# Kernel optimization log

Hardware: AMD Instinct MI355X
Metric: run time of the kernel (lower is better)

## Reference

```python
import jax, jax.numpy as jnp
import numpy as np

# 3 blocks x dilations [1..128] -> 24 residual layers, receptive field ~765
DILATIONS = tuple([1, 2, 4, 8, 16, 32, 64, 128] * 3)
WAVEFORM_BITS = 8


def setup_inputs() -> dict:
    key = jax.random.key(0)
    ks = jax.random.split(key, 8)
    B, C, S, K = 64, 64, 256, 256
    L = len(DILATIONS)
    s = 0.1  # keep gated activations away from saturation
    return {
        "waveform_seed": jax.random.randint(ks[0], (B, 1, 1), 0, K, dtype=jnp.int32),
        "embed": jax.random.normal(ks[1], (K, C), jnp.float32) * s,
        "conv_k": jax.random.normal(ks[2], (L, 2, C, 2 * C), jnp.float32) * s,  # [layer, tap(last/cur), C_in, 2C]
        "conv_b": jnp.zeros((L, 2 * C), jnp.float32),
        "res_w": jax.random.normal(ks[3], (L, C, C), jnp.float32) * s,
        "res_b": jnp.zeros((L, C), jnp.float32),
        "skip_w": jax.random.normal(ks[4], (L, C, S), jnp.float32) * s,
        "skip_b": jnp.zeros((L, S), jnp.float32),
        "out0_w": jax.random.normal(ks[5], (S, K), jnp.float32) * s,
        "out0_b": jnp.zeros((K,), jnp.float32),
        "out1_w": jax.random.normal(ks[6], (K, K), jnp.float32) * s,
        "out1_b": jnp.zeros((K,), jnp.float32),
        "max_infer_samples": 128,
    }


def _generate(seed, embed, conv_k, conv_b, res_w, res_b, skip_w, skip_b,
              out0_w, out0_b, out1_w, out1_b, T):
    B = seed.shape[0]
    C = embed.shape[1]
    sample0 = seed.reshape(B)
    # one circular-buffer queue per layer, length = dilation rate, zero-initialized
    queues0 = tuple(jnp.zeros((d, B, C), embed.dtype) for d in DILATIONS)

    def body(carry, _):
        t, sample, queues = carry
        x_cur = embed[sample]  # [B, C] embedding lookup of previous sample
        skip_sum = jnp.zeros((B, skip_w.shape[-1]), embed.dtype)
        new_queues = []
        for i, d in enumerate(DILATIONS):
            q = queues[i]
            pos = t % d  # circular buffer position == queue pop(0)/append semantics
            x_last = q[pos]
            new_queues.append(q.at[pos].set(x_cur))
            # kernel-size-2 dilated causal conv at a single step == two GEMMs
            h = x_last @ conv_k[i, 0] + x_cur @ conv_k[i, 1] + conv_b[i]  # [B, 2C]
            g = jnp.tanh(h[:, :C]) * jax.nn.sigmoid(h[:, C:])  # gated activation
            x_cur = x_cur + g @ res_w[i] + res_b[i]  # residual out
            skip_sum = skip_sum + g @ skip_w[i] + skip_b[i]  # skip connection
        h0 = jax.nn.relu(skip_sum @ out0_w + out0_b)
        logits = h0 @ out1_w + out1_b  # [B, K]
        nxt = jnp.argmax(logits, axis=-1).astype(jnp.int32)  # deterministic sampling
        return (t + 1, nxt, tuple(new_queues)), (nxt, logits)

    _, (samples, logits) = jax.lax.scan(
        body, (jnp.int32(0), sample0, queues0), None, length=T)
    return samples.transpose(1, 0), logits.transpose(1, 0, 2)  # [B,T], [B,T,K]


def reference(waveform_seed, embed, conv_k, conv_b, res_w, res_b, skip_w, skip_b,
              out0_w, out0_b, out1_w, out1_b, max_infer_samples):
    samples, logits = _generate(waveform_seed, embed, conv_k, conv_b, res_w, res_b,
                                skip_w, skip_b, out0_w, out0_b, out1_w, out1_b,
                                max_infer_samples)
    K = embed.shape[0]
    miu = float(K - 1)
    # rev quantize: map class in [0, 2^bits-1] back to [-1, 1]
    miu_wav = 2.0 * samples.astype(jnp.float32) / (2.0 ** WAVEFORM_BITS - 1.0) - 1.0
    # rev mu-law companding
    pred_wav = jnp.sign(miu_wav) * ((1.0 + miu) ** jnp.abs(miu_wav) - 1.0) / miu
    return pred_wav, logits
```

## Files before the change

### kernel.cpp

```cpp
#include <hip/hip_runtime.h>
#include <math.h>

#define NL 24
#define NB 64
#define TPB 512
#define QROWS 765
#define QFLOATS ((size_t)NB * QROWS * 64)
#define PACKW_F4 ((size_t)NL * 8 * 18 * 64)

typedef float vf4 __attribute__((ext_vector_type(4)));

struct WBc  { float4 v[8];  };
struct WBrs { float4 v[10]; };

__device__ __forceinline__ float hadd4(float4 v) { return (v.x + v.y) + (v.z + v.w); }
__device__ __forceinline__ void fma4(float4& a, float4 x, float4 w) {
    a.x = fmaf(x.x, w.x, a.x); a.y = fmaf(x.y, w.y, a.y);
    a.z = fmaf(x.z, w.z, a.z); a.w = fmaf(x.w, w.w, a.w);
}

__device__ __forceinline__ void bar() {
    asm volatile("s_waitcnt lgkmcnt(0)" ::: "memory");
    __builtin_amdgcn_s_barrier();
    asm volatile("" ::: "memory");
}

__device__ __forceinline__ void pf_c(WBc& b, const float4* __restrict__ packW, int i, int w, int l) {
    const float4* p = packW + ((size_t)(i * 8 + w) * 18) * 64 + l;
#pragma unroll
    for (int j = 0; j < 8; ++j) b.v[j] = p[j * 64];
}
__device__ __forceinline__ void pf_rs(WBrs& b, const float4* __restrict__ packW, int i, int w, int l) {
    const float4* p = packW + ((size_t)(i * 8 + w) * 18) * 64 + l;
#pragma unroll
    for (int j = 0; j < 10; ++j) b.v[j] = p[(8 + j) * 64];
}

__global__ void repack(const float* __restrict__ conv_k, const float* __restrict__ res_w,
                       const float* __restrict__ skip_w, const float* __restrict__ out0_w,
                       const float* __restrict__ out1_w, float* __restrict__ ws) {
    const int l = threadIdx.x;
    const int bb = blockIdx.x;
    float4* packW = (float4*)(ws + QFLOATS);
    float4* packH = packW + PACKW_F4;
    if (bb < NL * 8) {
        const int i = bb >> 3, w = bb & 7;
        float4* dst = packW + (size_t)bb * 18 * 64 + l;
        const int c  = w * 8 + (l & 7);
        const int kb = (l >> 3) * 16;
#pragma unroll
        for (int j = 0; j < 4; ++j) {
            float4 v;
            int k0 = kb + j * 4;
            v.x = conv_k[(((size_t)i * 2 + ((k0+0) >> 6)) * 64 + ((k0+0) & 63)) * 128 + c];
            v.y = conv_k[(((size_t)i * 2 + ((k0+1) >> 6)) * 64 + ((k0+1) & 63)) * 128 + c];
            v.z = conv_k[(((size_t)i * 2 + ((k0+2) >> 6)) * 64 + ((k0+2) & 63)) * 128 + c];
            v.w = conv_k[(((size_t)i * 2 + ((k0+3) >> 6)) * 64 + ((k0+3) & 63)) * 128 + c];
            dst[j * 64] = v;
        }
#pragma unroll
        for (int j = 0; j < 4; ++j) {
            float4 v;
            int k0 = kb + j * 4; int c2 = c + 64;
            v.x = conv_k[(((size_t)i * 2 + ((k0+0) >> 6)) * 64 + ((k0+0) & 63)) * 128 + c2];
            v.y = conv_k[(((size_t)i * 2 + ((k0+1) >> 6)) * 64 + ((k0+1) & 63)) * 128 + c2];
            v.z = conv_k[(((size_t)i * 2 + ((k0+2) >> 6)) * 64 + ((k0+2) & 63)) * 128 + c2];
            v.w = conv_k[(((size_t)i * 2 + ((k0+3) >> 6)) * 64 + ((k0+3) & 63)) * 128 + c2];
            dst[(4 + j) * 64] = v;
        }
        const int kr = (l >> 3) * 8;
#pragma unroll
        for (int j = 0; j < 2; ++j) {
            float4 v; int k0 = kr + j * 4;
            v.x = res_w[((size_t)i * 64 + k0 + 0) * 64 + c];
            v.y = res_w[((size_t)i * 64 + k0 + 1) * 64 + c];
            v.z = res_w[((size_t)i * 64 + k0 + 2) * 64 + c];
            v.w = res_w[((size_t)i * 64 + k0 + 3) * 64 + c];
            dst[(8 + j) * 64] = v;
        }
        const int s0 = w * 32 + (l & 15) * 2;
        const int ks = (l >> 4) * 16;
#pragma unroll
        for (int j = 0; j < 4; ++j) {
            float4 v; int k0 = ks + j * 4;
            v.x = skip_w[((size_t)i * 64 + k0 + 0) * 256 + s0];
            v.y = skip_w[((size_t)i * 64 + k0 + 1) * 256 + s0];
            v.z = skip_w[((size_t)i * 64 + k0 + 2) * 256 + s0];
            v.w = skip_w[((size_t)i * 64 + k0 + 3) * 256 + s0];
            dst[(10 + j) * 64] = v;
        }
#pragma unroll
        for (int j = 0; j < 4; ++j) {
            float4 v; int k0 = ks + j * 4; int s1 = s0 + 1;
            v.x = skip_w[((size_t)i * 64 + k0 + 0) * 256 + s1];
            v.y = skip_w[((size_t)i * 64 + k0 + 1) * 256 + s1];
            v.z = skip_w[((size_t)i * 64 + k0 + 2) * 256 + s1];
            v.w = skip_w[((size_t)i * 64 + k0 + 3) * 256 + s1];
            dst[(14 + j) * 64] = v;
        }
    } else {
        const int hb = bb - NL * 8;
        const int which = hb >> 3, w = hb & 7;
        const float* W = which ? out1_w : out0_w;
        float4* dst = packH + (size_t)hb * 32 * 64 + l;
        const int c  = w * 32 + (l & 31);
        const int kb = (l >> 5) * 128;
        for (int j = 0; j < 32; ++j) {
            float4 v; int k0 = kb + j * 4;
            v.x = W[(size_t)(k0 + 0) * 256 + c];
            v.y = W[(size_t)(k0 + 1) * 256 + c];
            v.z = W[(size_t)(k0 + 2) * 256 + c];
            v.w = W[(size_t)(k0 + 3) * 256 + c];
            dst[j * 64] = v;
        }
    }
}

__global__ __launch_bounds__(TPB, 1)
void wavenet_gen(const int* __restrict__ seed,
                 const float* __restrict__ embed,
                 const float* __restrict__ conv_b,
                 const float* __restrict__ res_b,
                 const float* __restrict__ skip_b,
                 const float* __restrict__ out0_b,
                 const float* __restrict__ out1_b,
                 const int* __restrict__ Tptr,
                 float* __restrict__ out,
                 float* __restrict__ ring,
                 const float4* __restrict__ packW,
                 const float4* __restrict__ packH)
{
    const int b   = blockIdx.x;
    const int tid = threadIdx.x;
    const int w   = tid >> 6;
    const int l   = tid & 63;
    const int T   = *Tptr;

    __shared__ __align__(16) float x2[128];
    __shared__ __align__(16) float gg[64];
    __shared__ __align__(16) float sk_lds[256];
    __shared__ __align__(16) float h0_lds[256];
    __shared__ __align__(16) float ebt[256 * 64];
    __shared__ __align__(16) float cb[NL * 128];
    __shared__ __align__(16) float rb[NL * 64];
    __shared__ __align__(16) float o0b[256], o1b[256];
    __shared__ __align__(16) float sbt[256];
    __shared__ float wmaxv[8];
    __shared__ int   wmaxi[8];

    float* q = ring + (size_t)b * (QROWS * 64);

    {
        vf4* q4 = (vf4*)q;
        const vf4 z = (vf4){0.f, 0.f, 0.f, 0.f};
        for (int idx = tid; idx < QROWS * 64 / 4; idx += TPB)
            __builtin_nontemporal_store(z, &q4[idx]);
        const float4* s4; float4* d4;
        s4 = (const float4*)embed;  d4 = (float4*)ebt;
        for (int idx = tid; idx < 256 * 64 / 4; idx += TPB) d4[idx] = s4[idx];
        s4 = (const float4*)conv_b; d4 = (float4*)cb;
        for (int idx = tid; idx < NL * 128 / 4; idx += TPB) d4[idx] = s4[idx];
        s4 = (const float4*)res_b;  d4 = (float4*)rb;
        for (int idx = tid; idx < NL * 64 / 4; idx += TPB) d4[idx] = s4[idx];
        s4 = (const float4*)out0_b; d4 = (float4*)o0b;
        for (int idx = tid; idx < 64; idx += TPB) d4[idx] = s4[idx];
        s4 = (const float4*)out1_b; d4 = (float4*)o1b;
        for (int idx = tid; idx < 64; idx += TPB) d4[idx] = s4[idx];
        if (tid < 256) {
            float acc = 0.f;
            for (int i = 0; i < NL; ++i) acc += skip_b[i * 256 + tid];
            sbt[tid] = acc;
        }
    }
    __syncthreads();
    if (tid < 64) {
        x2[tid] = 0.f;
        const int smp = seed[b];
        x2[64 + tid] = ebt[smp * 64 + tid];
    }
    __syncthreads();

    WBc  C0, C1;
    WBrs RS;
    pf_c(C0, packW, 0, w, l);

    float* out_pred = out + (size_t)b * T;
    float* out_log  = out + (size_t)NB * T + (size_t)b * T * 256;

    const int c   = w * 8 + (l & 7);
    const int kb  = (l >> 3) * 16;
    const int kr  = (l >> 3) * 8;
    const int ks  = (l >> 4) * 16;
    const int s0  = w * 32 + (l & 15) * 2;
    const int c2  = w * 32 + (l & 31);
    const int kb2 = (l >> 5) * 128;

    for (int t = 0; t < T; ++t) {
        float skv0 = 0.f, skv1 = 0.f;

        auto layer = [&](WBc& cur, WBc& nxt, const int i) {
            const int inx = (i + 1 < NL) ? (i + 1) : 0;
            pf_rs(RS, packW, i, w, l);
            pf_c(nxt, packW, inx, w, l);
            float xlnext = 0.f;
            if (w == 7) {
                const int d2 = 1 << (inx & 7);
                const int row2 = 255 * (inx >> 3) + (d2 - 1) + (t & (d2 - 1));
                xlnext = __builtin_nontemporal_load(&q[(size_t)row2 * 64 + l]);
            }
            if (w == 6) {
                const int d = 1 << (i & 7);
                const int row = 255 * (i >> 3) + (d - 1) + (t & (d - 1));
                __builtin_nontemporal_store(x2[64 + l], &q[(size_t)row * 64 + l]);
            }
            float4 xk0 = *(const float4*)&x2[kb];
            float4 xk1 = *(const float4*)&x2[kb + 4];
            float4 xk2 = *(const float4*)&x2[kb + 8];
            float4 xk3 = *(const float4*)&x2[kb + 12];
            float4 aA = make_float4(0.f, 0.f, 0.f, 0.f);
            float4 aB = make_float4(0.f, 0.f, 0.f, 0.f);
            fma4(aA, xk0, cur.v[0]); fma4(aA, xk1, cur.v[1]);
            fma4(aA, xk2, cur.v[2]); fma4(aA, xk3, cur.v[3]);
            fma4(aB, xk0, cur.v[4]); fma4(aB, xk1, cur.v[5]);
            fma4(aB, xk2, cur.v[6]); fma4(aB, xk3, cur.v[7]);
            float hA = hadd4(aA), hB = hadd4(aB);
            hA += __shfl_xor(hA, 8);  hB += __shfl_xor(hB, 8);
            hA += __shfl_xor(hA, 16); hB += __shfl_xor(hB, 16);
            hA += __shfl_xor(hA, 32); hB += __shfl_xor(hB, 32);
            hA += cb[i * 128 + c];
            hB += cb[i * 128 + 64 + c];
            const float g = tanhf(hA) * (1.f / (1.f + expf(-hB)));
            if (l < 8) gg[w * 8 + l] = g;
            bar();
            float4 gr0 = *(const float4*)&gg[kr];
            float4 gr1 = *(const float4*)&gg[kr + 4];
            float4 ra = make_float4(0.f, 0.f, 0.f, 0.f);
            fma4(ra, gr0, RS.v[0]); fma4(ra, gr1, RS.v[1]);
            float racc = hadd4(ra);
            racc += __shfl_xor(racc, 8);
            racc += __shfl_xor(racc, 16);
            racc += __shfl_xor(racc, 32);
            const float xnew = x2[64 + c] + racc + rb[i * 64 + c];
            float4 gs0 = *(const float4*)&gg[ks];
            float4 gs1 = *(const float4*)&gg[ks + 4];
            float4 gs2 = *(const float4*)&gg[ks + 8];
            float4 gs3 = *(const float4*)&gg[ks + 12];
            float4 sa0 = make_float4(0.f, 0.f, 0.f, 0.f);
            float4 sa1 = make_float4(0.f, 0.f, 0.f, 0.f);
            fma4(sa0, gs0, RS.v[2]); fma4(sa0, gs1, RS.v[3]);
            fma4(sa0, gs2, RS.v[4]); fma4(sa0, gs3, RS.v[5]);
            fma4(sa1, gs0, RS.v[6]); fma4(sa1, gs1, RS.v[7]);
            fma4(sa1, gs2, RS.v[8]); fma4(sa1, gs3, RS.v[9]);
            float ss0 = hadd4(sa0), ss1 = hadd4(sa1);
            ss0 += __shfl_xor(ss0, 16); ss1 += __shfl_xor(ss1, 16);
            ss0 += __shfl_xor(ss0, 32); ss1 += __shfl_xor(ss1, 32);
            skv0 += ss0;
            skv1 += ss1;
            if (l < 8) x2[64 + w * 8 + l] = xnew;
            if (w == 7) x2[l] = xlnext;
            bar();
        };

#pragma unroll 1
        for (int ii = 0; ii < NL; ii += 2) {
            layer(C0, C1, ii);
            layer(C1, C0, ii + 1);
        }

        if (l < 16) { sk_lds[s0] = skv0 + sbt[s0]; sk_lds[s0 + 1] = skv1 + sbt[s0 + 1]; }
        bar();
        {
            const float4* hp = packH + ((size_t)w * 32) * 64 + l;
            float4 ha = make_float4(0.f, 0.f, 0.f, 0.f);
#pragma unroll 8
            for (int cc = 0; cc < 32; ++cc) {
                float4 wv = hp[cc * 64];
                float4 sv = *(const float4*)&sk_lds[kb2 + cc * 4];
                fma4(ha, sv, wv);
            }
            float hs = hadd4(ha);
            hs += __shfl_xor(hs, 32);
            const float h0 = fmaxf(hs + o0b[c2], 0.f);
            if (l < 32) h0_lds[c2] = h0;
        }
        bar();
        float logit;
        {
            const float4* hp = packH + ((size_t)(8 + w) * 32) * 64 + l;
            float4 la = make_float4(0.f, 0.f, 0.f, 0.f);
#pragma unroll 8
            for (int cc = 0; cc < 32; ++cc) {
                float4 wv = hp[cc * 64];
                float4 hv = *(const float4*)&h0_lds[kb2 + cc * 4];
                fma4(la, hv, wv);
            }
            float ls = hadd4(la);
            ls += __shfl_xor(ls, 32);
            logit = ls + o1b[c2];
            if (l < 32)
                __builtin_nontemporal_store(logit, &out_log[(size_t)t * 256 + c2]);
        }
        {
            float bv = logit; int bi = c2;
#pragma unroll
            for (int off = 1; off <= 16; off <<= 1) {
                const float ov = __shfl_xor(bv, off);
                const int   oi = __shfl_xor(bi, off);
                if (ov > bv || (ov == bv && oi < bi)) { bv = ov; bi = oi; }
            }
            if (l == 0) { wmaxv[w] = bv; wmaxi[w] = bi; }
        }
        bar();
        {
            float fv = wmaxv[0]; int fi = wmaxi[0];
#pragma unroll
            for (int ww = 1; ww < 8; ++ww) {
                const float vv = wmaxv[ww]; const int vi = wmaxi[ww];
                if (vv > fv || (vv == fv && vi < fi)) { fv = vv; fi = vi; }
            }
            if (tid < 64) x2[64 + tid] = ebt[fi * 64 + tid];
            if (tid == 0) {
                const float mw = (float)fi * (2.0f / 255.0f) - 1.0f;
                const float a  = fabsf(mw);
                const float p  = (exp2f(8.0f * a) - 1.0f) * (1.0f / 255.0f);
                __builtin_nontemporal_store((mw < 0.f) ? -p : p, &out_pred[t]);
            }
        }
        bar();
    }
}

extern "C" void kernel_launch(void* const* d_in, const int* in_sizes, int n_in,
                              void* d_out, int out_size, void* d_ws, size_t ws_size,
                              hipStream_t stream) {
    const int*   seed   = (const int*)  d_in[0];
    const float* embed  = (const float*)d_in[1];
    const float* conv_k = (const float*)d_in[2];
    const float* conv_b = (const float*)d_in[3];
    const float* res_w  = (const float*)d_in[4];
    const float* res_b  = (const float*)d_in[5];
    const float* skip_w = (const float*)d_in[6];
    const float* skip_b = (const float*)d_in[7];
    const float* out0_w = (const float*)d_in[8];
    const float* out0_b = (const float*)d_in[9];
    const float* out1_w = (const float*)d_in[10];
    const float* out1_b = (const float*)d_in[11];
    const int*   Tptr   = (const int*)  d_in[12];

    float* ws = (float*)d_ws;
    float* ring = ws;
    const float4* packW = (const float4*)(ws + QFLOATS);
    const float4* packH = packW + PACKW_F4;

    repack<<<dim3(NL * 8 + 16), dim3(64), 0, stream>>>(
        conv_k, res_w, skip_w, out0_w, out1_w, ws);

    wavenet_gen<<<dim3(NB), dim3(TPB), 0, stream>>>(
        seed, embed, conv_b, res_b, skip_b, out0_b, out1_b, Tptr,
        (float*)d_out, ring, packW, packH);
}
```

Baseline: 6.379 ms.

## Fold residual projection into next layer's conv to halve per-layer barriers

```diff
diff --git a/kernel.cpp b/kernel.cpp
--- a/kernel.cpp
+++ b/kernel.cpp
@@ -5,12 +5,16 @@
 #define NB 64
 #define TPB 512
 #define QROWS 765
-#define QFLOATS ((size_t)NB * QROWS * 64)
-#define PACKW_F4 ((size_t)NL * 8 * 18 * 64)
+#define RING_F  3133440
+#define MB_OFF  RING_F
+#define CB2_OFF (MB_OFF + 24*64*128)
+#define CV_OFF  (CB2_OFF + 24*128)
+#define RS_OFF  (CV_OFF + 24*512*48)
+#define PH_OFF  (RS_OFF + 24*512*40)
 
 typedef float vf4 __attribute__((ext_vector_type(4)));
 
-struct WBc  { float4 v[8];  };
+struct WBc  { float4 v[12]; };
 struct WBrs { float4 v[10]; };
 
 __device__ __forceinline__ float hadd4(float4 v) { return (v.x + v.y) + (v.z + v.w); }
@@ -18,95 +22,128 @@
     a.x = fmaf(x.x, w.x, a.x); a.y = fmaf(x.y, w.y, a.y);
     a.z = fmaf(x.z, w.z, a.z); a.w = fmaf(x.w, w.w, a.w);
 }
-
 __device__ __forceinline__ void bar() {
     asm volatile("s_waitcnt lgkmcnt(0)" ::: "memory");
     __builtin_amdgcn_s_barrier();
     asm volatile("" ::: "memory");
 }
-
-__device__ __forceinline__ void pf_c(WBc& b, const float4* __restrict__ packW, int i, int w, int l) {
-    const float4* p = packW + ((size_t)(i * 8 + w) * 18) * 64 + l;
-#pragma unroll
-    for (int j = 0; j < 8; ++j) b.v[j] = p[j * 64];
-}
-__device__ __forceinline__ void pf_rs(WBrs& b, const float4* __restrict__ packW, int i, int w, int l) {
-    const float4* p = packW + ((size_t)(i * 8 + w) * 18) * 64 + l;
-#pragma unroll
-    for (int j = 0; j < 10; ++j) b.v[j] = p[(8 + j) * 64];
-}
-
-__global__ void repack(const float* __restrict__ conv_k, const float* __restrict__ res_w,
-                       const float* __restrict__ skip_w, const float* __restrict__ out0_w,
-                       const float* __restrict__ out1_w, float* __restrict__ ws) {
-    const int l = threadIdx.x;
-    const int bb = blockIdx.x;
-    float4* packW = (float4*)(ws + QFLOATS);
-    float4* packH = packW + PACKW_F4;
-    if (bb < NL * 8) {
-        const int i = bb >> 3, w = bb & 7;
-        float4* dst = packW + (size_t)bb * 18 * 64 + l;
+__device__ __forceinline__ void pf_cv(WBc& b, const float4* __restrict__ cvp, int layer, int tid) {
+    const float4* p = cvp + (size_t)layer * (12 * 512) + tid;
+#pragma unroll
+    for (int j = 0; j < 12; ++j) b.v[j] = p[j * 512];
+}
+__device__ __forceinline__ void pf_rs(WBrs& b, const float4* __restrict__ rsp, int layer, int tid) {
+    const float4* p = rsp + (size_t)layer * (10 * 512) + tid;
+#pragma unroll
+    for (int j = 0; j < 10; ++j) b.v[j] = p[j * 512];
+}
+
+__global__ void repack1(const float* __restrict__ conv_k, const float* __restrict__ res_w,
+                        const float* __restrict__ conv_b, const float* __restrict__ res_b,
+                        float* __restrict__ ws) {
+    const int i = blockIdx.x, col = threadIdx.x;
+    float* M   = ws + MB_OFF;
+    float* cb2 = ws + CB2_OFF;
+    if (i == 0) {
+        for (int m = 0; m < 64; ++m) M[(size_t)m * 128 + col] = 0.f;
+        cb2[col] = conv_b[col];
+        return;
+    }
+    float k1[64];
+#pragma unroll
+    for (int k = 0; k < 64; ++k)
+        k1[k] = conv_k[((size_t)(i * 2 + 1) * 64 + k) * 128 + col];
+    for (int m = 0; m < 64; ++m) {
+        float a = 0.f;
+#pragma unroll
+        for (int k = 0; k < 64; ++k)
+            a = fmaf(res_w[((size_t)(i - 1) * 64 + m) * 64 + k], k1[k], a);
+        M[((size_t)i * 64 + m) * 128 + col] = a;
+    }
+    float cb = conv_b[i * 128 + col];
+#pragma unroll
+    for (int k = 0; k < 64; ++k)
+        cb = fmaf(res_b[(i - 1) * 64 + k], k1[k], cb);
+    cb2[i * 128 + col] = cb;
+}
+
+__global__ void repack2(const float* __restrict__ conv_k, const float* __restrict__ res_w,
+                        const float* __restrict__ skip_w, const float* __restrict__ out0_w,
+                        const float* __restrict__ out1_w, float* __restrict__ ws) {
+    const int bb = blockIdx.x, tid = threadIdx.x;
+    float4* CV = (float4*)(ws + CV_OFF);
+    float4* RS = (float4*)(ws + RS_OFF);
+    float4* PH = (float4*)(ws + PH_OFF);
+    const float* M = ws + MB_OFF;
+    if (bb < NL) {
+        const int i = bb, w = tid >> 6, l = tid & 63;
         const int c  = w * 8 + (l & 7);
-        const int kb = (l >> 3) * 16;
-#pragma unroll
-        for (int j = 0; j < 4; ++j) {
-            float4 v;
-            int k0 = kb + j * 4;
-            v.x = conv_k[(((size_t)i * 2 + ((k0+0) >> 6)) * 64 + ((k0+0) & 63)) * 128 + c];
-            v.y = conv_k[(((size_t)i * 2 + ((k0+1) >> 6)) * 64 + ((k0+1) & 63)) * 128 + c];
-            v.z = conv_k[(((size_t)i * 2 + ((k0+2) >> 6)) * 64 + ((k0+2) & 63)) * 128 + c];
-            v.w = conv_k[(((size_t)i * 2 + ((k0+3) >> 6)) * 64 + ((k0+3) & 63)) * 128 + c];
-            dst[j * 64] = v;
-        }
-#pragma unroll
-        for (int j = 0; j < 4; ++j) {
-            float4 v;
-            int k0 = kb + j * 4; int c2 = c + 64;
-            v.x = conv_k[(((size_t)i * 2 + ((k0+0) >> 6)) * 64 + ((k0+0) & 63)) * 128 + c2];
-            v.y = conv_k[(((size_t)i * 2 + ((k0+1) >> 6)) * 64 + ((k0+1) & 63)) * 128 + c2];
-            v.z = conv_k[(((size_t)i * 2 + ((k0+2) >> 6)) * 64 + ((k0+2) & 63)) * 128 + c2];
-            v.w = conv_k[(((size_t)i * 2 + ((k0+3) >> 6)) * 64 + ((k0+3) & 63)) * 128 + c2];
-            dst[(4 + j) * 64] = v;
-        }
-        const int kr = (l >> 3) * 8;
-#pragma unroll
-        for (int j = 0; j < 2; ++j) {
-            float4 v; int k0 = kr + j * 4;
-            v.x = res_w[((size_t)i * 64 + k0 + 0) * 64 + c];
-            v.y = res_w[((size_t)i * 64 + k0 + 1) * 64 + c];
-            v.z = res_w[((size_t)i * 64 + k0 + 2) * 64 + c];
-            v.w = res_w[((size_t)i * 64 + k0 + 3) * 64 + c];
-            dst[(8 + j) * 64] = v;
+        const int k0 = (l >> 3) * 8;
+        float4* dst = CV + (size_t)i * (12 * 512) + tid;
+#pragma unroll
+        for (int half = 0; half < 2; ++half) {
+            const int cc = c + half * 64;
+#pragma unroll
+            for (int jj = 0; jj < 2; ++jj) {
+                const int kk = k0 + jj * 4;
+                float4 a, b, m;
+                a.x = conv_k[((size_t)(i * 2 + 0) * 64 + kk + 0) * 128 + cc];
+                a.y = conv_k[((size_t)(i * 2 + 0) * 64 + kk + 1) * 128 + cc];
+                a.z = conv_k[((size_t)(i * 2 + 0) * 64 + kk + 2) * 128 + cc];
+                a.w = conv_k[((size_t)(i * 2 + 0) * 64 + kk + 3) * 128 + cc];
+                b.x = conv_k[((size_t)(i * 2 + 1) * 64 + kk + 0) * 128 + cc];
+                b.y = conv_k[((size_t)(i * 2 + 1) * 64 + kk + 1) * 128 + cc];
+                b.z = conv_k[((size_t)(i * 2 + 1) * 64 + kk + 2) * 128 + cc];
+                b.w = conv_k[((size_t)(i * 2 + 1) * 64 + kk + 3) * 128 + cc];
+                m.x = M[((size_t)i * 64 + kk + 0) * 128 + cc];
+                m.y = M[((size_t)i * 64 + kk + 1) * 128 + cc];
+                m.z = M[((size_t)i * 64 + kk + 2) * 128 + cc];
+                m.w = M[((size_t)i * 64 + kk + 3) * 128 + cc];
+                dst[(half * 6 + 0 + jj) * 512] = a;
+                dst[(half * 6 + 2 + jj) * 512] = b;
+                dst[(half * 6 + 4 + jj) * 512] = m;
+            }
+        }
+        float4* rdst = RS + (size_t)i * (10 * 512) + tid;
+#pragma unroll
+        for (int jj = 0; jj < 2; ++jj) {
+            float4 v; const int kk = k0 + jj * 4;
+            v.x = res_w[((size_t)i * 64 + kk + 0) * 64 + c];
+            v.y = res_w[((size_t)i * 64 + kk + 1) * 64 + c];
+            v.z = res_w[((size_t)i * 64 + kk + 2) * 64 + c];
+            v.w = res_w[((size_t)i * 64 + kk + 3) * 64 + c];
+            rdst[jj * 512] = v;
         }
         const int s0 = w * 32 + (l & 15) * 2;
         const int ks = (l >> 4) * 16;
 #pragma unroll
-        for (int j = 0; j < 4; ++j) {
-            float4 v; int k0 = ks + j * 4;
-            v.x = skip_w[((size_t)i * 64 + k0 + 0) * 256 + s0];
-            v.y = skip_w[((size_t)i * 64 + k0 + 1) * 256 + s0];
-            v.z = skip_w[((size_t)i * 64 + k0 + 2) * 256 + s0];
-            v.w = skip_w[((size_t)i * 64 + k0 + 3) * 256 + s0];
-            dst[(10 + j) * 64] = v;
-        }
-#pragma unroll
-        for (int j = 0; j < 4; ++j) {
-            float4 v; int k0 = ks + j * 4; int s1 = s0 + 1;
-            v.x = skip_w[((size_t)i * 64 + k0 + 0) * 256 + s1];
-            v.y = skip_w[((size_t)i * 64 + k0 + 1) * 256 + s1];
-            v.z = skip_w[((size_t)i * 64 + k0 + 2) * 256 + s1];
-            v.w = skip_w[((size_t)i * 64 + k0 + 3) * 256 + s1];
-            dst[(14 + j) * 64] = v;
+        for (int jj = 0; jj < 4; ++jj) {
+            float4 v; const int kk = ks + jj * 4;
+            v.x = skip_w[((size_t)i * 64 + kk + 0) * 256 + s0];
+            v.y = skip_w[((size_t)i * 64 + kk + 1) * 256 + s0];
+            v.z = skip_w[((size_t)i * 64 + kk + 2) * 256 + s0];
+            v.w = skip_w[((size_t)i * 64 + kk + 3) * 256 + s0];
+            rdst[(2 + jj) * 512] = v;
+        }
+#pragma unroll
+        for (int jj = 0; jj < 4; ++jj) {
+            float4 v; const int kk = ks + jj * 4; const int s1 = s0 + 1;
+            v.x = skip_w[((size_t)i * 64 + kk + 0) * 256 + s1];
+            v.y = skip_w[((size_t)i * 64 + kk + 1) * 256 + s1];
+            v.z = skip_w[((size_t)i * 64 + kk + 2) * 256 + s1];
+            v.w = skip_w[((size_t)i * 64 + kk + 3) * 256 + s1];
+            rdst[(6 + jj) * 512] = v;
         }
     } else {
-        const int hb = bb - NL * 8;
-        const int which = hb >> 3, w = hb & 7;
+        if (tid >= 64) return;
+        const int hb = bb - NL;
+        const int which = hb >> 3, w = hb & 7, l = tid;
         const float* W = which ? out1_w : out0_w;
-        float4* dst = packH + (size_t)hb * 32 * 64 + l;
+        float4* dst = PH + (size_t)hb * (32 * 64) + l;
         const int c  = w * 32 + (l & 31);
         const int kb = (l >> 5) * 128;
         for (int j = 0; j < 32; ++j) {
-            float4 v; int k0 = kb + j * 4;
+            float4 v; const int k0 = kb + j * 4;
             v.x = W[(size_t)(k0 + 0) * 256 + c];
             v.y = W[(size_t)(k0 + 1) * 256 + c];
             v.z = W[(size_t)(k0 + 2) * 256 + c];
@@ -119,7 +156,6 @@
 __global__ __launch_bounds__(TPB, 1)
 void wavenet_gen(const int* __restrict__ seed,
                  const float* __restrict__ embed,
-                 const float* __restrict__ conv_b,
                  const float* __restrict__ res_b,
                  const float* __restrict__ skip_b,
                  const float* __restrict__ out0_b,
@@ -127,8 +163,10 @@
                  const int* __restrict__ Tptr,
                  float* __restrict__ out,
                  float* __restrict__ ring,
-                 const float4* __restrict__ packW,
-                 const float4* __restrict__ packH)
+                 const float4* __restrict__ cvp,
+                 const float4* __restrict__ rsp,
+                 const float4* __restrict__ php,
+                 const float* __restrict__ cb2p)
 {
     const int b   = blockIdx.x;
     const int tid = threadIdx.x;
@@ -136,15 +174,15 @@
     const int l   = tid & 63;
     const int T   = *Tptr;
 
-    __shared__ __align__(16) float x2[128];
-    __shared__ __align__(16) float gg[64];
-    __shared__ __align__(16) float sk_lds[256];
-    __shared__ __align__(16) float h0_lds[256];
+    __shared__ __align__(16) float xl[2][64];
+    __shared__ __align__(16) float yb[2][64];
+    __shared__ __align__(16) float gb[2][64];
+    __shared__ __align__(16) float skl[256];
+    __shared__ __align__(16) float h0l[256];
     __shared__ __align__(16) float ebt[256 * 64];
-    __shared__ __align__(16) float cb[NL * 128];
-    __shared__ __align__(16) float rb[NL * 64];
-    __shared__ __align__(16) float o0b[256], o1b[256];
-    __shared__ __align__(16) float sbt[256];
+    __shared__ __align__(16) float cb2S[NL * 128];
+    __shared__ __align__(16) float rbS[NL * 64];
+    __shared__ __align__(16) float o0bS[256], o1bS[256], sbtS[256];
     __shared__ float wmaxv[8];
     __shared__ int   wmaxi[8];
 
@@ -158,93 +196,132 @@
         const float4* s4; float4* d4;
         s4 = (const float4*)embed;  d4 = (float4*)ebt;
         for (int idx = tid; idx < 256 * 64 / 4; idx += TPB) d4[idx] = s4[idx];
-        s4 = (const float4*)conv_b; d4 = (float4*)cb;
+        s4 = (const float4*)cb2p;   d4 = (float4*)cb2S;
         for (int idx = tid; idx < NL * 128 / 4; idx += TPB) d4[idx] = s4[idx];
-        s4 = (const float4*)res_b;  d4 = (float4*)rb;
+        s4 = (const float4*)res_b;  d4 = (float4*)rbS;
         for (int idx = tid; idx < NL * 64 / 4; idx += TPB) d4[idx] = s4[idx];
-        s4 = (const float4*)out0_b; d4 = (float4*)o0b;
+        s4 = (const float4*)out0_b; d4 = (float4*)o0bS;
         for (int idx = tid; idx < 64; idx += TPB) d4[idx] = s4[idx];
-        s4 = (const float4*)out1_b; d4 = (float4*)o1b;
+        s4 = (const float4*)out1_b; d4 = (float4*)o1bS;
         for (int idx = tid; idx < 64; idx += TPB) d4[idx] = s4[idx];
         if (tid < 256) {
             float acc = 0.f;
             for (int i = 0; i < NL; ++i) acc += skip_b[i * 256 + tid];
-            sbt[tid] = acc;
+            sbtS[tid] = acc;
         }
     }
     __syncthreads();
     if (tid < 64) {
-        x2[tid] = 0.f;
         const int smp = seed[b];
-        x2[64 + tid] = ebt[smp * 64 + tid];
+        yb[0][tid] = ebt[smp * 64 + tid];
+        yb[1][tid] = 0.f;
+        xl[0][tid] = 0.f;
+        xl[1][tid] = 0.f;
+        gb[0][tid] = 0.f;
+        gb[1][tid] = 0.f;
     }
     __syncthreads();
 
-    WBc  C0, C1;
+    WBc  CVa, CVb;
     WBrs RS;
-    pf_c(C0, packW, 0, w, l);
+    pf_cv(CVa, cvp, 0, tid);
 
     float* out_pred = out + (size_t)b * T;
     float* out_log  = out + (size_t)NB * T + (size_t)b * T * 256;
 
     const int c   = w * 8 + (l & 7);
-    const int kb  = (l >> 3) * 16;
-    const int kr  = (l >> 3) * 8;
+    const int k0  = (l >> 3) * 8;
     const int ks  = (l >> 4) * 16;
     const int s0  = w * 32 + (l & 15) * 2;
     const int c2  = w * 32 + (l & 31);
     const int kb2 = (l >> 5) * 128;
 
+    float skv0 = 0.f, skv1 = 0.f;
+
     for (int t = 0; t < T; ++t) {
-        float skv0 = 0.f, skv1 = 0.f;
-
-        auto layer = [&](WBc& cur, WBc& nxt, const int i) {
-            const int inx = (i + 1 < NL) ? (i + 1) : 0;
-            pf_rs(RS, packW, i, w, l);
-            pf_c(nxt, packW, inx, w, l);
-            float xlnext = 0.f;
+
+        auto phase = [&](WBc& cur, WBc& nxt, const int i) {
+            const int j = (i + 1 < NL) ? (i + 1) : 0;
+            float xln = 0.f;
             if (w == 7) {
-                const int d2 = 1 << (inx & 7);
-                const int row2 = 255 * (inx >> 3) + (d2 - 1) + (t & (d2 - 1));
-                xlnext = __builtin_nontemporal_load(&q[(size_t)row2 * 64 + l]);
-            }
-            if (w == 6) {
-                const int d = 1 << (i & 7);
-                const int row = 255 * (i >> 3) + (d - 1) + (t & (d - 1));
-                __builtin_nontemporal_store(x2[64 + l], &q[(size_t)row * 64 + l]);
-            }
-            float4 xk0 = *(const float4*)&x2[kb];
-            float4 xk1 = *(const float4*)&x2[kb + 4];
-            float4 xk2 = *(const float4*)&x2[kb + 8];
-            float4 xk3 = *(const float4*)&x2[kb + 12];
+                const int dj = 1 << (j & 7);
+                const int s  = (i == NL - 1) ? (t + 1) : t;
+                const int row = 255 * (j >> 3) + (dj - 1) + (s & (dj - 1));
+                xln = __builtin_nontemporal_load(&q[(size_t)row * 64 + l]);
+            }
+            if (i) pf_rs(RS, rsp, i - 1, tid);
+            pf_cv(nxt, cvp, j, tid);
+            if (w == 6 && i) {
+                const int dp = 1 << ((i - 1) & 7);
+                const int row = 255 * ((i - 1) >> 3) + (dp - 1) + (t & (dp - 1));
+                __builtin_nontemporal_store(yb[(i - 1) & 1][l], &q[(size_t)row * 64 + l]);
+            }
+            const int ybi = i ? ((i - 1) & 1) : 0;
+            const int gbi = (i - 1) & 1;
+            const float4 xl0 = *(const float4*)&xl[i & 1][k0];
+            const float4 xl1 = *(const float4*)&xl[i & 1][k0 + 4];
+            const float4 yp0 = *(const float4*)&yb[ybi][k0];
+            const float4 yp1 = *(const float4*)&yb[ybi][k0 + 4];
+            const float4 gp0 = *(const float4*)&gb[gbi][k0];
+            const float4 gp1 = *(const float4*)&gb[gbi][k0 + 4];
             float4 aA = make_float4(0.f, 0.f, 0.f, 0.f);
             float4 aB = make_float4(0.f, 0.f, 0.f, 0.f);
-            fma4(aA, xk0, cur.v[0]); fma4(aA, xk1, cur.v[1]);
-            fma4(aA, xk2, cur.v[2]); fma4(aA, xk3, cur.v[3]);
-            fma4(aB, xk0, cur.v[4]); fma4(aB, xk1, cur.v[5]);
-            fma4(aB, xk2, cur.v[6]); fma4(aB, xk3, cur.v[7]);
+            fma4(aA, xl0, cur.v[0]); fma4(aA, xl1, cur.v[1]);
+            fma4(aA, yp0, cur.v[2]); fma4(aA, yp1, cur.v[3]);
+            fma4(aA, gp0, cur.v[4]); fma4(aA, gp1, cur.v[5]);
+            fma4(aB, xl0, cur.v[6]); fma4(aB, xl1, cur.v[7]);
+            fma4(aB, yp0, cur.v[8]); fma4(aB, yp1, cur.v[9]);
+            fma4(aB, gp0, cur.v[10]); fma4(aB, gp1, cur.v[11]);
             float hA = hadd4(aA), hB = hadd4(aB);
             hA += __shfl_xor(hA, 8);  hB += __shfl_xor(hB, 8);
             hA += __shfl_xor(hA, 16); hB += __shfl_xor(hB, 16);
             hA += __shfl_xor(hA, 32); hB += __shfl_xor(hB, 32);
-            hA += cb[i * 128 + c];
-            hB += cb[i * 128 + 64 + c];
+            hA += cb2S[i * 128 + c];
+            hB += cb2S[i * 128 + 64 + c];
             const float g = tanhf(hA) * (1.f / (1.f + expf(-hB)));
-            if (l < 8) gg[w * 8 + l] = g;
+            float ynew = 0.f;
+            if (i) {
+                float4 ra = make_float4(0.f, 0.f, 0.f, 0.f);
+                fma4(ra, gp0, RS.v[0]); fma4(ra, gp1, RS.v[1]);
+                float racc = hadd4(ra);
+                racc += __shfl_xor(racc, 8);
+                racc += __shfl_xor(racc, 16);
+                racc += __shfl_xor(racc, 32);
+                ynew = yb[ybi][c] + racc + rbS[(i - 1) * 64 + c];
+                const float4 gs0 = *(const float4*)&gb[gbi][ks];
+                const float4 gs1 = *(const float4*)&gb[gbi][ks + 4];
+                const float4 gs2 = *(const float4*)&gb[gbi][ks + 8];
+                const float4 gs3 = *(const float4*)&gb[gbi][ks + 12];
+                float4 sa0 = make_float4(0.f, 0.f, 0.f, 0.f);
+                float4 sa1 = make_float4(0.f, 0.f, 0.f, 0.f);
+                fma4(sa0, gs0, RS.v[2]); fma4(sa0, gs1, RS.v[3]);
+                fma4(sa0, gs2, RS.v[4]); fma4(sa0, gs3, RS.v[5]);
+                fma4(sa1, gs0, RS.v[6]); fma4(sa1, gs1, RS.v[7]);
+                fma4(sa1, gs2, RS.v[8]); fma4(sa1, gs3, RS.v[9]);
+                float ss0 = hadd4(sa0), ss1 = hadd4(sa1);
+                ss0 += __shfl_xor(ss0, 16); ss1 += __shfl_xor(ss1, 16);
+                ss0 += __shfl_xor(ss0, 32); ss1 += __shfl_xor(ss1, 32);
+                skv0 += ss0;
+                skv1 += ss1;
+            }
+            if (l < 8) gb[i & 1][w * 8 + l] = g;
+            if (i && l < 8) yb[i & 1][w * 8 + l] = ynew;
+            if (w == 7) xl[j & 1][l] = xln;
             bar();
-            float4 gr0 = *(const float4*)&gg[kr];
-            float4 gr1 = *(const float4*)&gg[kr + 4];
-            float4 ra = make_float4(0.f, 0.f, 0.f, 0.f);
-            fma4(ra, gr0, RS.v[0]); fma4(ra, gr1, RS.v[1]);
-            float racc = hadd4(ra);
-            racc += __shfl_xor(racc, 8);
-            racc += __shfl_xor(racc, 16);
-            racc += __shfl_xor(racc, 32);
-            const float xnew = x2[64 + c] + racc + rb[i * 64 + c];
-            float4 gs0 = *(const float4*)&gg[ks];
-            float4 gs1 = *(const float4*)&gg[ks + 4];
-            float4 gs2 = *(const float4*)&gg[ks + 8];
-            float4 gs3 = *(const float4*)&gg[ks + 12];
+        };
+
+#pragma unroll 1
+        for (int ii = 0; ii < NL; ii += 2) {
+            phase(CVa, CVb, ii);
+            phase(CVb, CVa, ii + 1);
+        }
+
+        {
+            pf_rs(RS, rsp, NL - 1, tid);
+            const float4 gs0 = *(const float4*)&gb[1][ks];
+            const float4 gs1 = *(const float4*)&gb[1][ks + 4];
+            const float4 gs2 = *(const float4*)&gb[1][ks + 8];
+            const float4 gs3 = *(const float4*)&gb[1][ks + 12];
             float4 sa0 = make_float4(0.f, 0.f, 0.f, 0.f);
             float4 sa1 = make_float4(0.f, 0.f, 0.f, 0.f);
             fma4(sa0, gs0, RS.v[2]); fma4(sa0, gs1, RS.v[3]);
@@ -256,51 +333,46 @@
             ss0 += __shfl_xor(ss0, 32); ss1 += __shfl_xor(ss1, 32);
             skv0 += ss0;
             skv1 += ss1;
-            if (l < 8) x2[64 + w * 8 + l] = xnew;
-            if (w == 7) x2[l] = xlnext;
+            if (l < 16) {
+                skl[s0] = skv0 + sbtS[s0];
+                skl[s0 + 1] = skv1 + sbtS[s0 + 1];
+            }
+            skv0 = 0.f; skv1 = 0.f;
+            if (w == 6) {
+                const int row = 510 + 127 + (t & 127);
+                __builtin_nontemporal_store(yb[1][l], &q[(size_t)row * 64 + l]);
+            }
             bar();
-        };
-
-#pragma unroll 1
-        for (int ii = 0; ii < NL; ii += 2) {
-            layer(C0, C1, ii);
-            layer(C1, C0, ii + 1);
-        }
-
-        if (l < 16) { sk_lds[s0] = skv0 + sbt[s0]; sk_lds[s0 + 1] = skv1 + sbt[s0 + 1]; }
-        bar();
+        }
         {
-            const float4* hp = packH + ((size_t)w * 32) * 64 + l;
+            const float4* hp = php + ((size_t)w * 32) * 64 + l;
             float4 ha = make_float4(0.f, 0.f, 0.f, 0.f);
 #pragma unroll 8
             for (int cc = 0; cc < 32; ++cc) {
                 float4 wv = hp[cc * 64];
-                float4 sv = *(const float4*)&sk_lds[kb2 + cc * 4];
+                float4 sv = *(const float4*)&skl[kb2 + cc * 4];
                 fma4(ha, sv, wv);
             }
             float hs = hadd4(ha);
             hs += __shfl_xor(hs, 32);
-            const float h0 = fmaxf(hs + o0b[c2], 0.f);
-            if (l < 32) h0_lds[c2] = h0;
+            const float h0 = fmaxf(hs + o0bS[c2], 0.f);
+            if (l < 32) h0l[c2] = h0;
         }
         bar();
-        float logit;
         {
-            const float4* hp = packH + ((size_t)(8 + w) * 32) * 64 + l;
+            const float4* hp = php + ((size_t)(8 + w) * 32) * 64 + l;
             float4 la = make_float4(0.f, 0.f, 0.f, 0.f);
 #pragma unroll 8
             for (int cc = 0; cc < 32; ++cc) {
                 float4 wv = hp[cc * 64];
-                float4 hv = *(const float4*)&h0_lds[kb2 + cc * 4];
+                float4 hv = *(const float4*)&h0l[kb2 + cc * 4];
                 fma4(la, hv, wv);
             }
             float ls = hadd4(la);
             ls += __shfl_xor(ls, 32);
-            logit = ls + o1b[c2];
+            const float logit = ls + o1bS[c2];
             if (l < 32)
                 __builtin_nontemporal_store(logit, &out_log[(size_t)t * 256 + c2]);
-        }
-        {
             float bv = logit; int bi = c2;
 #pragma unroll
             for (int off = 1; off <= 16; off <<= 1) {
@@ -318,7 +390,7 @@
                 const float vv = wmaxv[ww]; const int vi = wmaxi[ww];
                 if (vv > fv || (vv == fv && vi < fi)) { fv = vv; fi = vi; }
             }
-            if (tid < 64) x2[64 + tid] = ebt[fi * 64 + tid];
+            if (tid < 64) yb[0][tid] = ebt[fi * 64 + tid];
             if (tid == 0) {
                 const float mw = (float)fi * (2.0f / 255.0f) - 1.0f;
                 const float a  = fabsf(mw);
@@ -349,13 +421,15 @@
 
     float* ws = (float*)d_ws;
     float* ring = ws;
-    const float4* packW = (const float4*)(ws + QFLOATS);
-    const float4* packH = packW + PACKW_F4;
-
-    repack<<<dim3(NL * 8 + 16), dim3(64), 0, stream>>>(
-        conv_k, res_w, skip_w, out0_w, out1_w, ws);
+    const float4* cvp  = (const float4*)(ws + CV_OFF);
+    const float4* rsp  = (const float4*)(ws + RS_OFF);
+    const float4* php  = (const float4*)(ws + PH_OFF);
+    const float*  cb2p = ws + CB2_OFF;
+
+    repack1<<<dim3(NL), dim3(128), 0, stream>>>(conv_k, res_w, conv_b, res_b, ws);
+    repack2<<<dim3(NL + 16), dim3(512), 0, stream>>>(conv_k, res_w, skip_w, out0_w, out1_w, ws);
 
     wavenet_gen<<<dim3(NB), dim3(TPB), 0, stream>>>(
-        seed, embed, conv_b, res_b, skip_b, out0_b, out1_b, Tptr,
-        (float*)d_out, ring, packW, packH);
-}
+        seed, embed, res_b, skip_b, out0_b, out1_b, Tptr,
+        (float*)d_out, ring, cvp, rsp, php, cb2p);
+}
```

New measurement: 7.919 ms. 24.1% more time.

## Defer skip-connection GEMMs out of the serial layer chain into one batched pass

Applied to the files above, without the earlier changes.

```diff
diff --git a/kernel.cpp b/kernel.cpp
--- a/kernel.cpp
+++ b/kernel.cpp
@@ -5,108 +5,103 @@
 #define NB 64
 #define TPB 512
 #define QROWS 765
-#define QFLOATS ((size_t)NB * QROWS * 64)
-#define PACKW_F4 ((size_t)NL * 8 * 18 * 64)
+#define RING_F  3133440
+#define CVP_OFF RING_F
+#define RP_OFF  (CVP_OFF + 24*8*512*4)
+#define SP_OFF  (RP_OFF  + 24*2*512*4)
+#define PH_OFF  (SP_OFF  + 24*8*512*4)
 
 typedef float vf4 __attribute__((ext_vector_type(4)));
 
-struct WBc  { float4 v[8];  };
-struct WBrs { float4 v[10]; };
+struct WBc { float4 v[8]; };
+struct WBr { float4 v[2]; };
+struct SWB { float4 v[8]; };
 
 __device__ __forceinline__ float hadd4(float4 v) { return (v.x + v.y) + (v.z + v.w); }
 __device__ __forceinline__ void fma4(float4& a, float4 x, float4 w) {
     a.x = fmaf(x.x, w.x, a.x); a.y = fmaf(x.y, w.y, a.y);
     a.z = fmaf(x.z, w.z, a.z); a.w = fmaf(x.w, w.w, a.w);
 }
-
 __device__ __forceinline__ void bar() {
     asm volatile("s_waitcnt lgkmcnt(0)" ::: "memory");
     __builtin_amdgcn_s_barrier();
     asm volatile("" ::: "memory");
 }
-
-__device__ __forceinline__ void pf_c(WBc& b, const float4* __restrict__ packW, int i, int w, int l) {
-    const float4* p = packW + ((size_t)(i * 8 + w) * 18) * 64 + l;
-#pragma unroll
-    for (int j = 0; j < 8; ++j) b.v[j] = p[j * 64];
-}
-__device__ __forceinline__ void pf_rs(WBrs& b, const float4* __restrict__ packW, int i, int w, int l) {
-    const float4* p = packW + ((size_t)(i * 8 + w) * 18) * 64 + l;
-#pragma unroll
-    for (int j = 0; j < 10; ++j) b.v[j] = p[(8 + j) * 64];
+__device__ __forceinline__ void pf_c(WBc& b, const float4* __restrict__ cvp, int i, int tid) {
+    const float4* p = cvp + (size_t)i * (8 * 512) + tid;
+#pragma unroll
+    for (int j = 0; j < 8; ++j) b.v[j] = p[j * 512];
+}
+__device__ __forceinline__ void pf_r(WBr& b, const float4* __restrict__ rp, int i, int tid) {
+    const float4* p = rp + (size_t)i * (2 * 512) + tid;
+#pragma unroll
+    for (int j = 0; j < 2; ++j) b.v[j] = p[j * 512];
+}
+__device__ __forceinline__ void pf_s(SWB& b, const float4* __restrict__ sp, int i, int tid) {
+    const float4* p = sp + (size_t)i * (8 * 512) + tid;
+#pragma unroll
+    for (int j = 0; j < 8; ++j) b.v[j] = p[j * 512];
 }
 
 __global__ void repack(const float* __restrict__ conv_k, const float* __restrict__ res_w,
                        const float* __restrict__ skip_w, const float* __restrict__ out0_w,
                        const float* __restrict__ out1_w, float* __restrict__ ws) {
-    const int l = threadIdx.x;
-    const int bb = blockIdx.x;
-    float4* packW = (float4*)(ws + QFLOATS);
-    float4* packH = packW + PACKW_F4;
-    if (bb < NL * 8) {
-        const int i = bb >> 3, w = bb & 7;
-        float4* dst = packW + (size_t)bb * 18 * 64 + l;
+    const int bb = blockIdx.x, tid = threadIdx.x;
+    float4* CVP = (float4*)(ws + CVP_OFF);
+    float4* RP  = (float4*)(ws + RP_OFF);
+    float4* SP  = (float4*)(ws + SP_OFF);
+    float4* PH  = (float4*)(ws + PH_OFF);
+    if (bb < NL) {
+        const int i = bb, w = tid >> 6, l = tid & 63;
         const int c  = w * 8 + (l & 7);
         const int kb = (l >> 3) * 16;
-#pragma unroll
-        for (int j = 0; j < 4; ++j) {
-            float4 v;
-            int k0 = kb + j * 4;
-            v.x = conv_k[(((size_t)i * 2 + ((k0+0) >> 6)) * 64 + ((k0+0) & 63)) * 128 + c];
-            v.y = conv_k[(((size_t)i * 2 + ((k0+1) >> 6)) * 64 + ((k0+1) & 63)) * 128 + c];
-            v.z = conv_k[(((size_t)i * 2 + ((k0+2) >> 6)) * 64 + ((k0+2) & 63)) * 128 + c];
-            v.w = conv_k[(((size_t)i * 2 + ((k0+3) >> 6)) * 64 + ((k0+3) & 63)) * 128 + c];
-            dst[j * 64] = v;
-        }
-#pragma unroll
-        for (int j = 0; j < 4; ++j) {
-            float4 v;
-            int k0 = kb + j * 4; int c2 = c + 64;
-            v.x = conv_k[(((size_t)i * 2 + ((k0+0) >> 6)) * 64 + ((k0+0) & 63)) * 128 + c2];
-            v.y = conv_k[(((size_t)i * 2 + ((k0+1) >> 6)) * 64 + ((k0+1) & 63)) * 128 + c2];
-            v.z = conv_k[(((size_t)i * 2 + ((k0+2) >> 6)) * 64 + ((k0+2) & 63)) * 128 + c2];
-            v.w = conv_k[(((size_t)i * 2 + ((k0+3) >> 6)) * 64 + ((k0+3) & 63)) * 128 + c2];
-            dst[(4 + j) * 64] = v;
+        float4* dst = CVP + (size_t)i * (8 * 512) + tid;
+#pragma unroll
+        for (int half = 0; half < 2; ++half) {
+            const int cc = c + half * 64;
+#pragma unroll
+            for (int j = 0; j < 4; ++j) {
+                float4 v; const int k0 = kb + j * 4;
+                v.x = conv_k[(((size_t)i * 2 + ((k0+0) >> 6)) * 64 + ((k0+0) & 63)) * 128 + cc];
+                v.y = conv_k[(((size_t)i * 2 + ((k0+1) >> 6)) * 64 + ((k0+1) & 63)) * 128 + cc];
+                v.z = conv_k[(((size_t)i * 2 + ((k0+2) >> 6)) * 64 + ((k0+2) & 63)) * 128 + cc];
+                v.w = conv_k[(((size_t)i * 2 + ((k0+3) >> 6)) * 64 + ((k0+3) & 63)) * 128 + cc];
+                dst[(half * 4 + j) * 512] = v;
+            }
         }
         const int kr = (l >> 3) * 8;
+        float4* rdst = RP + (size_t)i * (2 * 512) + tid;
 #pragma unroll
         for (int j = 0; j < 2; ++j) {
-            float4 v; int k0 = kr + j * 4;
+            float4 v; const int k0 = kr + j * 4;
             v.x = res_w[((size_t)i * 64 + k0 + 0) * 64 + c];
             v.y = res_w[((size_t)i * 64 + k0 + 1) * 64 + c];
             v.z = res_w[((size_t)i * 64 + k0 + 2) * 64 + c];
             v.w = res_w[((size_t)i * 64 + k0 + 3) * 64 + c];
-            dst[(8 + j) * 64] = v;
-        }
-        const int s0 = w * 32 + (l & 15) * 2;
-        const int ks = (l >> 4) * 16;
-#pragma unroll
-        for (int j = 0; j < 4; ++j) {
-            float4 v; int k0 = ks + j * 4;
-            v.x = skip_w[((size_t)i * 64 + k0 + 0) * 256 + s0];
-            v.y = skip_w[((size_t)i * 64 + k0 + 1) * 256 + s0];
-            v.z = skip_w[((size_t)i * 64 + k0 + 2) * 256 + s0];
-            v.w = skip_w[((size_t)i * 64 + k0 + 3) * 256 + s0];
-            dst[(10 + j) * 64] = v;
-        }
-#pragma unroll
-        for (int j = 0; j < 4; ++j) {
-            float4 v; int k0 = ks + j * 4; int s1 = s0 + 1;
-            v.x = skip_w[((size_t)i * 64 + k0 + 0) * 256 + s1];
-            v.y = skip_w[((size_t)i * 64 + k0 + 1) * 256 + s1];
-            v.z = skip_w[((size_t)i * 64 + k0 + 2) * 256 + s1];
-            v.w = skip_w[((size_t)i * 64 + k0 + 3) * 256 + s1];
-            dst[(14 + j) * 64] = v;
+            rdst[j * 512] = v;
+        }
+        const int s  = tid >> 1;
+        const int kh = (tid & 1) * 32;
+        float4* sdst = SP + (size_t)i * (8 * 512) + tid;
+#pragma unroll
+        for (int j = 0; j < 8; ++j) {
+            float4 v; const int k0 = kh + j * 4;
+            v.x = skip_w[((size_t)i * 64 + k0 + 0) * 256 + s];
+            v.y = skip_w[((size_t)i * 64 + k0 + 1) * 256 + s];
+            v.z = skip_w[((size_t)i * 64 + k0 + 2) * 256 + s];
+            v.w = skip_w[((size_t)i * 64 + k0 + 3) * 256 + s];
+            sdst[j * 512] = v;
         }
     } else {
-        const int hb = bb - NL * 8;
-        const int which = hb >> 3, w = hb & 7;
+        if (tid >= 64) return;
+        const int hb = bb - NL;
+        const int which = hb >> 3, w = hb & 7, l = tid;
         const float* W = which ? out1_w : out0_w;
-        float4* dst = packH + (size_t)hb * 32 * 64 + l;
+        float4* dst = PH + (size_t)hb * (32 * 64) + l;
         const int c  = w * 32 + (l & 31);
         const int kb = (l >> 5) * 128;
         for (int j = 0; j < 32; ++j) {
-            float4 v; int k0 = kb + j * 4;
+            float4 v; const int k0 = kb + j * 4;
             v.x = W[(size_t)(k0 + 0) * 256 + c];
             v.y = W[(size_t)(k0 + 1) * 256 + c];
             v.z = W[(size_t)(k0 + 2) * 256 + c];
@@ -127,8 +122,10 @@
                  const int* __restrict__ Tptr,
                  float* __restrict__ out,
                  float* __restrict__ ring,
-                 const float4* __restrict__ packW,
-                 const float4* __restrict__ packH)
+                 const float4* __restrict__ cvp,
+                 const float4* __restrict__ rp,
+                 const float4* __restrict__ sp,
+                 const float4* __restrict__ php)
 {
     const int b   = blockIdx.x;
     const int tid = threadIdx.x;
@@ -137,14 +134,13 @@
     const int T   = *Tptr;
 
     __shared__ __align__(16) float x2[128];
-    __shared__ __align__(16) float gg[64];
-    __shared__ __align__(16) float sk_lds[256];
-    __shared__ __align__(16) float h0_lds[256];
+    __shared__ __align__(16) float gAll[NL * 64];
+    __shared__ __align__(16) float skl[256];
+    __shared__ __align__(16) float h0l[256];
     __shared__ __align__(16) float ebt[256 * 64];
     __shared__ __align__(16) float cb[NL * 128];
-    __shared__ __align__(16) float rb[NL * 64];
-    __shared__ __align__(16) float o0b[256], o1b[256];
-    __shared__ __align__(16) float sbt[256];
+    __shared__ __align__(16) float rbS[NL * 64];
+    __shared__ __align__(16) float o0b[256], o1b[256], sbt[256];
     __shared__ float wmaxv[8];
     __shared__ int   wmaxi[8];
 
@@ -160,7 +156,7 @@
         for (int idx = tid; idx < 256 * 64 / 4; idx += TPB) d4[idx] = s4[idx];
         s4 = (const float4*)conv_b; d4 = (float4*)cb;
         for (int idx = tid; idx < NL * 128 / 4; idx += TPB) d4[idx] = s4[idx];
-        s4 = (const float4*)res_b;  d4 = (float4*)rb;
+        s4 = (const float4*)res_b;  d4 = (float4*)rbS;
         for (int idx = tid; idx < NL * 64 / 4; idx += TPB) d4[idx] = s4[idx];
         s4 = (const float4*)out0_b; d4 = (float4*)o0b;
         for (int idx = tid; idx < 64; idx += TPB) d4[idx] = s4[idx];
@@ -180,9 +176,9 @@
     }
     __syncthreads();
 
-    WBc  C0, C1;
-    WBrs RS;
-    pf_c(C0, packW, 0, w, l);
+    WBc CVa, CVb;
+    WBr RS;
+    pf_c(CVa, cvp, 0, tid);
 
     float* out_pred = out + (size_t)b * T;
     float* out_log  = out + (size_t)NB * T + (size_t)b * T * 256;
@@ -190,18 +186,17 @@
     const int c   = w * 8 + (l & 7);
     const int kb  = (l >> 3) * 16;
     const int kr  = (l >> 3) * 8;
-    const int ks  = (l >> 4) * 16;
-    const int s0  = w * 32 + (l & 15) * 2;
+    const int sc  = tid >> 1;
+    const int kh  = (tid & 1) * 32;
     const int c2  = w * 32 + (l & 31);
     const int kb2 = (l >> 5) * 128;
 
     for (int t = 0; t < T; ++t) {
-        float skv0 = 0.f, skv1 = 0.f;
 
         auto layer = [&](WBc& cur, WBc& nxt, const int i) {
             const int inx = (i + 1 < NL) ? (i + 1) : 0;
-            pf_rs(RS, packW, i, w, l);
-            pf_c(nxt, packW, inx, w, l);
+            pf_r(RS, rp, i, tid);
+            if (inx) pf_c(nxt, cvp, inx, tid);
             float xlnext = 0.f;
             if (w == 7) {
                 const int d2 = 1 << (inx & 7);
@@ -230,32 +225,17 @@
             hA += cb[i * 128 + c];
             hB += cb[i * 128 + 64 + c];
             const float g = tanhf(hA) * (1.f / (1.f + expf(-hB)));
-            if (l < 8) gg[w * 8 + l] = g;
+            if (l < 8) gAll[i * 64 + w * 8 + l] = g;
             bar();
-            float4 gr0 = *(const float4*)&gg[kr];
-            float4 gr1 = *(const float4*)&gg[kr + 4];
+            float4 gr0 = *(const float4*)&gAll[i * 64 + kr];
+            float4 gr1 = *(const float4*)&gAll[i * 64 + kr + 4];
             float4 ra = make_float4(0.f, 0.f, 0.f, 0.f);
             fma4(ra, gr0, RS.v[0]); fma4(ra, gr1, RS.v[1]);
             float racc = hadd4(ra);
             racc += __shfl_xor(racc, 8);
             racc += __shfl_xor(racc, 16);
             racc += __shfl_xor(racc, 32);
-            const float xnew = x2[64 + c] + racc + rb[i * 64 + c];
-            float4 gs0 = *(const float4*)&gg[ks];
-            float4 gs1 = *(const float4*)&gg[ks + 4];
-            float4 gs2 = *(const float4*)&gg[ks + 8];
-            float4 gs3 = *(const float4*)&gg[ks + 12];
-            float4 sa0 = make_float4(0.f, 0.f, 0.f, 0.f);
-            float4 sa1 = make_float4(0.f, 0.f, 0.f, 0.f);
-            fma4(sa0, gs0, RS.v[2]); fma4(sa0, gs1, RS.v[3]);
-            fma4(sa0, gs2, RS.v[4]); fma4(sa0, gs3, RS.v[5]);
-            fma4(sa1, gs0, RS.v[6]); fma4(sa1, gs1, RS.v[7]);
-            fma4(sa1, gs2, RS.v[8]); fma4(sa1, gs3, RS.v[9]);
-            float ss0 = hadd4(sa0), ss1 = hadd4(sa1);
-            ss0 += __shfl_xor(ss0, 16); ss1 += __shfl_xor(ss1, 16);
-            ss0 += __shfl_xor(ss0, 32); ss1 += __shfl_xor(ss1, 32);
-            skv0 += ss0;
-            skv1 += ss1;
+            const float xnew = x2[64 + c] + racc + rbS[i * 64 + c];
             if (l < 8) x2[64 + w * 8 + l] = xnew;
             if (w == 7) x2[l] = xlnext;
             bar();
@@ -263,35 +243,63 @@
 
 #pragma unroll 1
         for (int ii = 0; ii < NL; ii += 2) {
-            layer(C0, C1, ii);
-            layer(C1, C0, ii + 1);
-        }
-
-        if (l < 16) { sk_lds[s0] = skv0 + sbt[s0]; sk_lds[s0 + 1] = skv1 + sbt[s0 + 1]; }
+            layer(CVa, CVb, ii);
+            layer(CVb, CVa, ii + 1);
+        }
+
+        {
+            SWB sA, sB;
+            pf_s(sA, sp, 0, tid);
+            float sk = 0.f;
+#pragma unroll
+            for (int ii = 0; ii < NL; ii += 2) {
+                pf_s(sB, sp, ii + 1, tid);
+                {
+                    const float* gi = &gAll[ii * 64 + kh];
+                    float4 acc = make_float4(0.f, 0.f, 0.f, 0.f);
+#pragma unroll
+                    for (int j = 0; j < 8; ++j)
+                        fma4(acc, *(const float4*)&gi[j * 4], sA.v[j]);
+                    sk += hadd4(acc);
+                }
+                if (ii + 2 < NL) pf_s(sA, sp, ii + 2, tid);
+                {
+                    const float* gi = &gAll[(ii + 1) * 64 + kh];
+                    float4 acc = make_float4(0.f, 0.f, 0.f, 0.f);
+#pragma unroll
+                    for (int j = 0; j < 8; ++j)
+                        fma4(acc, *(const float4*)&gi[j * 4], sB.v[j]);
+                    sk += hadd4(acc);
+                }
+            }
+            sk += __shfl_xor(sk, 1);
+            if ((tid & 1) == 0) skl[sc] = sk + sbt[sc];
+        }
         bar();
         {
-            const float4* hp = packH + ((size_t)w * 32) * 64 + l;
+            const float4* hp = php + ((size_t)w * 32) * 64 + l;
             float4 ha = make_float4(0.f, 0.f, 0.f, 0.f);
 #pragma unroll 8
             for (int cc = 0; cc < 32; ++cc) {
                 float4 wv = hp[cc * 64];
-                float4 sv = *(const float4*)&sk_lds[kb2 + cc * 4];
+                float4 sv = *(const float4*)&skl[kb2 + cc * 4];
                 fma4(ha, sv, wv);
             }
             float hs = hadd4(ha);
             hs += __shfl_xor(hs, 32);
             const float h0 = fmaxf(hs + o0b[c2], 0.f);
-            if (l < 32) h0_lds[c2] = h0;
+            if (l < 32) h0l[c2] = h0;
         }
         bar();
+        pf_c(CVa, cvp, 0, tid);
         float logit;
         {
-            const float4* hp = packH + ((size_t)(8 + w) * 32) * 64 + l;
+            const float4* hp = php + ((size_t)(8 + w) * 32) * 64 + l;
             float4 la = make_float4(0.f, 0.f, 0.f, 0.f);
 #pragma unroll 8
             for (int cc = 0; cc < 32; ++cc) {
                 float4 wv = hp[cc * 64];
-                float4 hv = *(const float4*)&h0_lds[kb2 + cc * 4];
+                float4 hv = *(const float4*)&h0l[kb2 + cc * 4];
                 fma4(la, hv, wv);
             }
             float ls = hadd4(la);
@@ -349,13 +357,15 @@
 
     float* ws = (float*)d_ws;
     float* ring = ws;
-    const float4* packW = (const float4*)(ws + QFLOATS);
-    const float4* packH = packW + PACKW_F4;
-
-    repack<<<dim3(NL * 8 + 16), dim3(64), 0, stream>>>(
+    const float4* cvp = (const float4*)(ws + CVP_OFF);
+    const float4* rp  = (const float4*)(ws + RP_OFF);
+    const float4* sp  = (const float4*)(ws + SP_OFF);
+    const float4* php = (const float4*)(ws + PH_OFF);
+
+    repack<<<dim3(NL + 16), dim3(TPB), 0, stream>>>(
         conv_k, res_w, skip_w, out0_w, out1_w, ws);
 
     wavenet_gen<<<dim3(NB), dim3(TPB), 0, stream>>>(
         seed, embed, conv_b, res_b, skip_b, out0_b, out1_b, Tptr,
-        (float*)d_out, ring, packW, packH);
-}
+        (float*)d_out, ring, cvp, rp, sp, php);
+}
```

New measurement: 12.75 ms. +99.9%, slower.
